# Optimization experiments

Hardware: AMD Instinct MI355X
Metric: run time of the kernel (lower is better)

Reference implementation:

```python
import jax, jax.numpy as jnp
import numpy as np

B, N, D = 8, 4096, 1024
NC, NU = 8, 32            # core / universal experts (num_experts=16, occ_factor=1/4)
E = NC + NU               # 40 total experts
S = 2                     # slots per expert
HC, HU = 4 * D, D         # core hidden = 4*dim, occ hidden = 4*occ_factor*dim = dim
L2_EPS = 1e-6
LN_EPS = 1e-5


def l2norm(x):
    n = jnp.sqrt(jnp.sum(x * x, axis=-1, keepdims=True))
    return x * (1.0 / (n + L2_EPS))


def layernorm(x, g, b):
    mu = jnp.mean(x, axis=-1, keepdims=True)
    var = jnp.mean((x - mu) ** 2, axis=-1, keepdims=True)
    return (x - mu) / jnp.sqrt(var + LN_EPS) * g + b


def entmax15(z):
    # exact 1.5-entmax over last axis (sorted algorithm, Peters et al. 2019)
    z = z / 2.0
    z = z - jnp.max(z, axis=-1, keepdims=True)
    zs = -jnp.sort(-z, axis=-1)                      # descending
    K = z.shape[-1]
    k = jnp.arange(1, K + 1, dtype=z.dtype)
    mean = jnp.cumsum(zs, axis=-1) / k
    meansq = jnp.cumsum(zs * zs, axis=-1) / k
    ss = k * (meansq - mean * mean)
    delta = jnp.maximum((1.0 - ss) / k, 1e-12)
    tau = mean - jnp.sqrt(delta)
    support = jnp.sum((tau <= zs).astype(jnp.int32), axis=-1, keepdims=True)
    tau_star = jnp.take_along_axis(tau, support - 1, axis=-1)
    return jnp.maximum(z - tau_star, 0.0) ** 2


def setup_inputs() -> dict:
    key = jax.random.key(0)
    ks = jax.random.split(key, 8)
    return {
        "x": jax.random.normal(ks[0], (B, N, D), jnp.float32),
        "attn_weight": jax.random.uniform(ks[1], (B, 128), jnp.float32),
        "phi": jax.random.normal(ks[2], (E, S, D), jnp.float32) * 0.02,
        "key_gamma": jnp.ones((D,), jnp.float32),
        "key_beta": jnp.zeros((D,), jnp.float32),
        "query_gamma": jnp.ones((D,), jnp.float32),
        "query_beta": jnp.zeros((D,), jnp.float32),
        "ln_gamma": jnp.ones((D,), jnp.float32),
        "ln_beta": jnp.zeros((D,), jnp.float32),
        "scale0": jnp.asarray(0.5, jnp.float32),
        "scale1": jnp.asarray(0.5, jnp.float32),
        "core_w1": jax.random.normal(ks[3], (NC, D, HC), jnp.float32) * (D ** -0.5),
        "core_b1": jnp.zeros((NC, HC), jnp.float32),
        "core_w2": jax.random.normal(ks[4], (NC, HC, D), jnp.float32) * (HC ** -0.5),
        "core_b2": jnp.zeros((NC, D), jnp.float32),
        "occ_w1": jax.random.normal(ks[5], (NU, D, HU), jnp.float32) * (D ** -0.5),
        "occ_b1": jnp.zeros((NU, HU), jnp.float32),
        "occ_w2": jax.random.normal(ks[6], (NU, HU, D), jnp.float32) * (HU ** -0.5),
        "occ_b2": jnp.zeros((NU, D), jnp.float32),
    }


def _expert_mlp(s, w1, b1, w2, b2):
    # s: [b, e, s, d]; per-expert 2-layer MLP with exact GELU
    h = jax.nn.gelu(jnp.einsum('besd,edh->besh', s, w1) + b1[None, :, None, :], approximate=False)
    return jnp.einsum('besh,ehd->besd', h, w2) + b2[None, :, None, :]


def reference(x, attn_weight, phi, key_gamma, key_beta, query_gamma, query_beta,
              ln_gamma, ln_beta, scale0, scale1,
              core_w1, core_b1, core_w2, core_b2,
              occ_w1, occ_b1, occ_w2, occ_b2):
    # keys: OffsetScale then l2norm
    k = l2norm(x * key_gamma + key_beta)
    # queries: OffsetScale -> LayerNorm -> l2norm on phi
    q = layernorm(phi * query_gamma + query_beta, ln_gamma, ln_beta)
    q = l2norm(q)
    logits = jnp.einsum('bnd,esd->bnes', k, q)                      # [B,N,E,S]
    core_mask = (jnp.arange(E) < NC)[None, None, :, None]
    adjusted = jnp.where(core_mask, logits, jnp.asarray(-10000.0, logits.dtype))
    dispatch = jax.nn.softmax(adjusted / scale0, axis=2)            # softmax over experts
    combine = entmax15((adjusted / scale1).reshape(B, N, E * S))    # [B,N,E*S]
    slots = jnp.einsum('bnd,bnes->besd', x, dispatch)               # [B,E,S,D]
    core_out = _expert_mlp(slots[:, :NC], core_w1, core_b1, core_w2, core_b2)
    occ_out = _expert_mlp(slots[:, NC:], occ_w1, occ_b1, occ_w2, occ_b2)
    out = jnp.concatenate([core_out, occ_out], axis=1).reshape(B, E * S, D)
    return jnp.einsum('bsd,bns->bnd', out, combine)                 # [B,N,D]
```

## Files before the change

### kernel.cpp

```cpp
#include <hip/hip_runtime.h>
#include <hip/hip_bf16.h>

#define B_ 8
#define N_ 4096
#define D_ 1024

#define AS1 __attribute__((address_space(1)))
#define AS3 __attribute__((address_space(3)))
__device__ __forceinline__ void gld16(const float* g, float* l) {
    __builtin_amdgcn_global_load_lds((const AS1 void*)g, (AS3 void*)l, 16, 0, 0);
}

__global__ __launch_bounds__(64) void k_prep(
    const float* __restrict__ phi, const float* __restrict__ qg, const float* __restrict__ qb,
    const float* __restrict__ lng, const float* __restrict__ lnb,
    const float* __restrict__ kg, const float* __restrict__ kb,
    float* __restrict__ qk, float* __restrict__ cj, float* __restrict__ wbuf)
{
    int r = blockIdx.x;
    int lane = threadIdx.x;
    if (r == 16) {
        float cacc = 0.f;
#pragma unroll
        for (int c = 0; c < 16; ++c) {
            int i = c * 64 + lane;
            float g = kg[i], b = kb[i];
            wbuf[i] = g * g;
            wbuf[1024 + i] = 2.0f * g * b;
            cacc += b * b;
        }
#pragma unroll
        for (int m = 32; m; m >>= 1) cacc += __shfl_xor(cacc, m);
        if (lane == 0) wbuf[2048] = cacc;
        return;
    }
    const float* pr = phi + (size_t)r * D_;
    float v[16];
    float s1 = 0.f;
#pragma unroll
    for (int c = 0; c < 16; ++c) {
        int i = c * 64 + lane;
        v[c] = pr[i] * qg[i] + qb[i];
        s1 += v[c];
    }
#pragma unroll
    for (int m = 32; m; m >>= 1) s1 += __shfl_xor(s1, m);
    float mu = s1 * (1.0f / D_);
    float s2 = 0.f;
#pragma unroll
    for (int c = 0; c < 16; ++c) { float dd = v[c] - mu; s2 += dd * dd; }
#pragma unroll
    for (int m = 32; m; m >>= 1) s2 += __shfl_xor(s2, m);
    float var = s2 * (1.0f / D_);
    float inv = 1.0f / sqrtf(var + 1e-5f);
    float u[16];
    float s3 = 0.f;
#pragma unroll
    for (int c = 0; c < 16; ++c) {
        int i = c * 64 + lane;
        u[c] = (v[c] - mu) * inv * lng[i] + lnb[i];
        s3 += u[c] * u[c];
    }
#pragma unroll
    for (int m = 32; m; m >>= 1) s3 += __shfl_xor(s3, m);
    float rn = 1.0f / (sqrtf(s3) + 1e-6f);
    float cacc = 0.f;
#pragma unroll
    for (int c = 0; c < 16; ++c) {
        int i = c * 64 + lane;
        float qv = u[c] * rn;
        qk[(size_t)r * D_ + i] = qv * kg[i];
        cacc += qv * kb[i];
    }
#pragma unroll
    for (int m = 32; m; m >>= 1) cacc += __shfl_xor(cacc, m);
    if (lane == 0) cj[r] = cacc;
}

__global__ __launch_bounds__(256) void k_logits(
    const float* __restrict__ x, const float* __restrict__ qk,
    const float* __restrict__ wbuf, float* __restrict__ lgbuf)
{
    __shared__ float smem[5248];
    float* xs  = smem;
    float* qs  = smem + 4096;
    float* wsd = smem + 5120;

    int tid = threadIdx.x;
    int tok0 = blockIdx.x * 64;
    int tok32 = tid & 31, gg = tid >> 5;
    int wid = tid >> 6;

    float acc[2][17];
#pragma unroll
    for (int u = 0; u < 2; ++u)
#pragma unroll
        for (int v = 0; v < 17; ++v) acc[u][v] = 0.f;

    int st[4], sg[4];
#pragma unroll
    for (int i = 0; i < 4; ++i) {
        int s = i * 256 + tid;
        int tok = s >> 4, sc = s & 15;
        st[i] = tok;
        sg[i] = (sc ^ (tok & 15)) << 2;
    }

#pragma unroll 1
    for (int dc = 0; dc < 16; ++dc) {
#pragma unroll
        for (int i = 0; i < 4; ++i)
            gld16(x + (size_t)(tok0 + st[i]) * D_ + dc * 64 + sg[i],
                  &xs[(i * 256 + wid * 64) * 4]);
        gld16(qk + (size_t)(tid >> 4) * D_ + dc * 64 + ((tid & 15) << 2),
              &qs[wid * 256]);
        if (tid < 128) wsd[tid] = wbuf[(size_t)(tid >> 6) * 1024 + dc * 64 + (tid & 63)];
        __syncthreads();

        const float* qp = qs + gg * 8;
        const float* wp = wsd + gg * 8;
#pragma unroll
        for (int dl4 = 0; dl4 < 2; ++dl4) {
            int c = gg * 2 + dl4;
            int t0 = tok32, t1 = 32 + tok32;
            float4 xv0 = *(const float4*)(&xs[(t0 * 16 + (c ^ (t0 & 15))) * 4]);
            float4 xv1 = *(const float4*)(&xs[(t1 * 16 + (c ^ (t1 & 15))) * 4]);
            float4 w2v = *(const float4*)(wp + dl4 * 4);
            float4 w1v = *(const float4*)(wp + 64 + dl4 * 4);
            acc[0][16] += (w2v.x * xv0.x + w1v.x) * xv0.x + (w2v.y * xv0.y + w1v.y) * xv0.y
                        + (w2v.z * xv0.z + w1v.z) * xv0.z + (w2v.w * xv0.w + w1v.w) * xv0.w;
            acc[1][16] += (w2v.x * xv1.x + w1v.x) * xv1.x + (w2v.y * xv1.y + w1v.y) * xv1.y
                        + (w2v.z * xv1.z + w1v.z) * xv1.z + (w2v.w * xv1.w + w1v.w) * xv1.w;
#pragma unroll
            for (int j = 0; j < 16; ++j) {
                float4 q4 = *(const float4*)(qp + j * 64 + dl4 * 4);
                acc[0][j] += xv0.x * q4.x + xv0.y * q4.y + xv0.z * q4.z + xv0.w * q4.w;
                acc[1][j] += xv1.x * q4.x + xv1.y * q4.y + xv1.z * q4.z + xv1.w * q4.w;
            }
        }
        __syncthreads();
    }

    float* red = smem;
#pragma unroll
    for (int half = 0; half < 2; ++half) {
        __syncthreads();
#pragma unroll
        for (int v = 0; v < 17; ++v) red[(tok32 * 17 + v) * 8 + gg] = acc[half][v];
        __syncthreads();
#pragma unroll
        for (int it = 0; it < 3; ++it) {
            int idx = tid + it * 256;
            if (idx < 544) {
                float4 p0 = *(const float4*)(red + idx * 8);
                float4 p1v = *(const float4*)(red + idx * 8 + 4);
                float sum = ((p0.x + p0.y) + (p0.z + p0.w)) + ((p1v.x + p1v.y) + (p1v.z + p1v.w));
                int t = idx / 17, v = idx - t * 17;
                lgbuf[(size_t)(tok0 + half * 32 + t) * 20 + v] = sum;
            }
        }
    }
}

__global__ __launch_bounds__(64) void k_epi(
    const float* __restrict__ lgbuf, const float* __restrict__ cj,
    const float* __restrict__ wbuf,
    const float* __restrict__ s0p, const float* __restrict__ s1p,
    float* __restrict__ combine, float* __restrict__ dispatch)
{
    int tok = blockIdx.x * 64 + threadIdx.x;
    const float* lp = lgbuf + (size_t)tok * 20;
    float s[17];
    float4 q0 = *(const float4*)(lp + 0);
    float4 q1 = *(const float4*)(lp + 4);
    float4 q2 = *(const float4*)(lp + 8);
    float4 q3 = *(const float4*)(lp + 12);
    s[0] = q0.x; s[1] = q0.y; s[2] = q0.z; s[3] = q0.w;
    s[4] = q1.x; s[5] = q1.y; s[6] = q1.z; s[7] = q1.w;
    s[8] = q2.x; s[9] = q2.y; s[10] = q2.z; s[11] = q2.w;
    s[12] = q3.x; s[13] = q3.y; s[14] = q3.z; s[15] = q3.w;
    s[16] = lp[16];

    float ss = s[16] + wbuf[2048];
    float rn = 1.0f / (sqrtf(ss) + 1e-6f);
    float inv0 = 1.0f / s0p[0];
    float inv1h = 0.5f / s1p[0];
    float lg[16];
#pragma unroll
    for (int j = 0; j < 16; ++j) lg[j] = (s[j] + cj[j]) * rn;

    float dsp[16];
#pragma unroll
    for (int sl = 0; sl < 2; ++sl) {
        float a[8], m = -1e30f;
#pragma unroll
        for (int ee = 0; ee < 8; ++ee) { a[ee] = lg[2 * ee + sl] * inv0; m = fmaxf(m, a[ee]); }
        float den = 0.f;
#pragma unroll
        for (int ee = 0; ee < 8; ++ee) { a[ee] = expf(a[ee] - m); den += a[ee]; }
        float r = 1.0f / den;
#pragma unroll
        for (int ee = 0; ee < 8; ++ee) dsp[2 * ee + sl] = a[ee] * r;
    }

    float z[16], zmax = -1e30f;
#pragma unroll
    for (int j = 0; j < 16; ++j) { z[j] = lg[j] * inv1h; zmax = fmaxf(zmax, z[j]); }
#pragma unroll
    for (int j = 0; j < 16; ++j) z[j] -= zmax;
    float zsr[16];
#pragma unroll
    for (int j = 0; j < 16; ++j) zsr[j] = z[j];
#pragma unroll
    for (int rr = 0; rr < 16; ++rr) {
#pragma unroll
        for (int jj = (rr & 1); jj + 1 < 16; jj += 2) {
            float aa = zsr[jj], bb = zsr[jj + 1];
            zsr[jj] = fmaxf(aa, bb);
            zsr[jj + 1] = fminf(aa, bb);
        }
    }
    float cs = 0.f, css = 0.f, tau_star = 0.f;
#pragma unroll
    for (int kk = 1; kk <= 16; ++kk) {
        cs += zsr[kk - 1];
        css += zsr[kk - 1] * zsr[kk - 1];
        float fk = (float)kk;
        float mean = cs / fk, msq = css / fk;
        float ssv = fk * (msq - mean * mean);
        float delta = fmaxf((1.0f - ssv) / fk, 1e-12f);
        float tau = mean - sqrtf(delta);
        tau_star = (tau <= zsr[kk - 1]) ? tau : tau_star;
    }
    float4* cw = (float4*)(combine + (size_t)tok * 16);
    float4* dw = (float4*)(dispatch + (size_t)tok * 16);
#pragma unroll
    for (int q4i = 0; q4i < 4; ++q4i) {
        float4 cv, dv;
        float t0 = fmaxf(z[q4i * 4 + 0] - tau_star, 0.f);
        float t1 = fmaxf(z[q4i * 4 + 1] - tau_star, 0.f);
        float t2 = fmaxf(z[q4i * 4 + 2] - tau_star, 0.f);
        float t3 = fmaxf(z[q4i * 4 + 3] - tau_star, 0.f);
        cv.x = t0 * t0; cv.y = t1 * t1; cv.z = t2 * t2; cv.w = t3 * t3;
        dv.x = dsp[q4i * 4 + 0]; dv.y = dsp[q4i * 4 + 1];
        dv.z = dsp[q4i * 4 + 2]; dv.w = dsp[q4i * 4 + 3];
        cw[q4i] = cv;
        dw[q4i] = dv;
    }
}

__global__ __launch_bounds__(256) void k_slots_partial(
    const float* __restrict__ x, const float* __restrict__ dispatch,
    float* __restrict__ spart)
{
    __shared__ float sm[1024];
    int nc = blockIdx.x, b = blockIdx.y;
    int tid = threadIdx.x;
    int n0 = nc * 64;
    ((float4*)sm)[tid] = ((const float4*)(dispatch + ((size_t)b * N_ + n0) * 16))[tid];
    __syncthreads();

    const float* xp = x + ((size_t)b * N_ + n0) * D_ + tid * 4;
    float4 acc[16];
#pragma unroll
    for (int j = 0; j < 16; ++j) { acc[j].x = 0.f; acc[j].y = 0.f; acc[j].z = 0.f; acc[j].w = 0.f; }
#pragma unroll 8
    for (int n = 0; n < 64; ++n) {
        float4 xv = *(const float4*)(xp + (size_t)n * D_);
        const float4* q4 = (const float4*)(sm + n * 16);
        float4 s0 = q4[0], s1 = q4[1], s2 = q4[2], s3 = q4[3];
        acc[0].x  += s0.x * xv.x; acc[0].y  += s0.x * xv.y; acc[0].z  += s0.x * xv.z; acc[0].w  += s0.x * xv.w;
        acc[1].x  += s0.y * xv.x; acc[1].y  += s0.y * xv.y; acc[1].z  += s0.y * xv.z; acc[1].w  += s0.y * xv.w;
        acc[2].x  += s0.z * xv.x; acc[2].y  += s0.z * xv.y; acc[2].z  += s0.z * xv.z; acc[2].w  += s0.z * xv.w;
        acc[3].x  += s0.w * xv.x; acc[3].y  += s0.w * xv.y; acc[3].z  += s0.w * xv.z; acc[3].w  += s0.w * xv.w;
        acc[4].x  += s1.x * xv.x; acc[4].y  += s1.x * xv.y; acc[4].z  += s1.x * xv.z; acc[4].w  += s1.x * xv.w;
        acc[5].x  += s1.y * xv.x; acc[5].y  += s1.y * xv.y; acc[5].z  += s1.y * xv.z; acc[5].w  += s1.y * xv.w;
        acc[6].x  += s1.z * xv.x; acc[6].y  += s1.z * xv.y; acc[6].z  += s1.z * xv.z; acc[6].w  += s1.z * xv.w;
        acc[7].x  += s1.w * xv.x; acc[7].y  += s1.w * xv.y; acc[7].z  += s1.w * xv.z; acc[7].w  += s1.w * xv.w;
        acc[8].x  += s2.x * xv.x; acc[8].y  += s2.x * xv.y; acc[8].z  += s2.x * xv.z; acc[8].w  += s2.x * xv.w;
        acc[9].x  += s2.y * xv.x; acc[9].y  += s2.y * xv.y; acc[9].z  += s2.y * xv.z; acc[9].w  += s2.y * xv.w;
        acc[10].x += s2.z * xv.x; acc[10].y += s2.z * xv.y; acc[10].z += s2.z * xv.z; acc[10].w += s2.z * xv.w;
        acc[11].x += s2.w * xv.x; acc[11].y += s2.w * xv.y; acc[11].z += s2.w * xv.z; acc[11].w += s2.w * xv.w;
        acc[12].x += s3.x * xv.x; acc[12].y += s3.x * xv.y; acc[12].z += s3.x * xv.z; acc[12].w += s3.x * xv.w;
        acc[13].x += s3.y * xv.x; acc[13].y += s3.y * xv.y; acc[13].z += s3.y * xv.z; acc[13].w += s3.y * xv.w;
        acc[14].x += s3.z * xv.x; acc[14].y += s3.z * xv.y; acc[14].z += s3.z * xv.z; acc[14].w += s3.z * xv.w;
        acc[15].x += s3.w * xv.x; acc[15].y += s3.w * xv.y; acc[15].z += s3.w * xv.z; acc[15].w += s3.w * xv.w;
    }
    float* op = spart + (((size_t)b * 64 + nc) * 16) * 1024 + tid * 4;
#pragma unroll
    for (int j = 0; j < 16; ++j)
        *(float4*)(op + (size_t)j * 1024) = acc[j];
}

__global__ __launch_bounds__(256) void k_slots_reduce(
    const float* __restrict__ spart, float* __restrict__ slotsT)
{
    int j = blockIdx.x, b = blockIdx.y;
    int tid = threadIdx.x;
    const float* p = spart + ((size_t)(b * 64) * 16 + j) * 1024 + tid * 4;
    float4 s; s.x = 0.f; s.y = 0.f; s.z = 0.f; s.w = 0.f;
#pragma unroll 8
    for (int nc = 0; nc < 64; ++nc) {
        float4 v = *(const float4*)(p + (size_t)nc * 16384);
        s.x += v.x; s.y += v.y; s.z += v.z; s.w += v.w;
    }
    int e = j >> 1, sl = j & 1;
    int t = b * 2 + sl;
    float* o = slotsT + ((size_t)e * 1024 + tid * 4) * 16 + t;
    o[0] = s.x; o[16] = s.y; o[32] = s.z; o[48] = s.w;
}

__global__ __launch_bounds__(256) void k_mlp1(
    const float* __restrict__ w1, const float* __restrict__ slotsT,
    float* __restrict__ p1)
{
    __shared__ float sm[1024];
    int cc = blockIdx.x, ks = blockIdx.y, e = blockIdx.z;
    int tid = threadIdx.x;
    int k0 = ks * 64;
    int col = cc * 1024 + tid * 4;
    ((float4*)sm)[tid] = ((const float4*)(slotsT + ((size_t)e * 1024 + k0) * 16))[tid];
    __syncthreads();

    const float* wp = w1 + (size_t)e * 1024 * 4096 + (size_t)k0 * 4096 + col;
    float4 acc[16];
#pragma unroll
    for (int t = 0; t < 16; ++t) { acc[t].x = 0.f; acc[t].y = 0.f; acc[t].z = 0.f; acc[t].w = 0.f; }
#pragma unroll 8
    for (int kk = 0; kk < 64; ++kk) {
        float4 w = *(const float4*)(wp + (size_t)kk * 4096);
        const float4* q4 = (const float4*)(sm + kk * 16);
        float4 s0 = q4[0], s1 = q4[1], s2 = q4[2], s3 = q4[3];
        acc[0].x  += s0.x * w.x; acc[0].y  += s0.x * w.y; acc[0].z  += s0.x * w.z; acc[0].w  += s0.x * w.w;
        acc[1].x  += s0.y * w.x; acc[1].y  += s0.y * w.y; acc[1].z  += s0.y * w.z; acc[1].w  += s0.y * w.w;
        acc[2].x  += s0.z * w.x; acc[2].y  += s0.z * w.y; acc[2].z  += s0.z * w.z; acc[2].w  += s0.z * w.w;
        acc[3].x  += s0.w * w.x; acc[3].y  += s0.w * w.y; acc[3].z  += s0.w * w.z; acc[3].w  += s0.w * w.w;
        acc[4].x  += s1.x * w.x; acc[4].y  += s1.x * w.y; acc[4].z  += s1.x * w.z; acc[4].w  += s1.x * w.w;
        acc[5].x  += s1.y * w.x; acc[5].y  += s1.y * w.y; acc[5].z  += s1.y * w.z; acc[5].w  += s1.y * w.w;
        acc[6].x  += s1.z * w.x; acc[6].y  += s1.z * w.y; acc[6].z  += s1.z * w.z; acc[6].w  += s1.z * w.w;
        acc[7].x  += s1.w * w.x; acc[7].y  += s1.w * w.y; acc[7].z  += s1.w * w.z; acc[7].w  += s1.w * w.w;
        acc[8].x  += s2.x * w.x; acc[8].y  += s2.x * w.y; acc[8].z  += s2.x * w.z; acc[8].w  += s2.x * w.w;
        acc[9].x  += s2.y * w.x; acc[9].y  += s2.y * w.y; acc[9].z  += s2.y * w.z; acc[9].w  += s2.y * w.w;
        acc[10].x += s2.z * w.x; acc[10].y += s2.z * w.y; acc[10].z += s2.z * w.z; acc[10].w += s2.z * w.w;
        acc[11].x += s2.w * w.x; acc[11].y += s2.w * w.y; acc[11].z += s2.w * w.z; acc[11].w += s2.w * w.w;
        acc[12].x += s3.x * w.x; acc[12].y += s3.x * w.y; acc[12].z += s3.x * w.z; acc[12].w += s3.x * w.w;
        acc[13].x += s3.y * w.x; acc[13].y += s3.y * w.y; acc[13].z += s3.y * w.z; acc[13].w += s3.y * w.w;
        acc[14].x += s3.z * w.x; acc[14].y += s3.z * w.y; acc[14].z += s3.z * w.z; acc[14].w += s3.z * w.w;
        acc[15].x += s3.w * w.x; acc[15].y += s3.w * w.y; acc[15].z += s3.w * w.z; acc[15].w += s3.w * w.w;
    }
    float av0[16], av1[16], av2[16], av3[16];
#pragma unroll
    for (int t = 0; t < 16; ++t) { av0[t] = acc[t].x; av1[t] = acc[t].y; av2[t] = acc[t].z; av3[t] = acc[t].w; }
    float* op = p1 + (((size_t)ks * 8 + e) * 4096 + col) * 16;
#pragma unroll
    for (int q = 0; q < 4; ++q) {
        *(float4*)(op + 0 * 16 + q * 4) = make_float4(av0[q*4+0], av0[q*4+1], av0[q*4+2], av0[q*4+3]);
        *(float4*)(op + 1 * 16 + q * 4) = make_float4(av1[q*4+0], av1[q*4+1], av1[q*4+2], av1[q*4+3]);
        *(float4*)(op + 2 * 16 + q * 4) = make_float4(av2[q*4+0], av2[q*4+1], av2[q*4+2], av2[q*4+3]);
        *(float4*)(op + 3 * 16 + q * 4) = make_float4(av3[q*4+0], av3[q*4+1], av3[q*4+2], av3[q*4+3]);
    }
}

__global__ __launch_bounds__(256) void k_mlp2f(
    const float* __restrict__ w2, const float* __restrict__ p1,
    const float* __restrict__ b1, float* __restrict__ p2)
{
    __shared__ float sm[1024];
    int ks = blockIdx.x, e = blockIdx.y;
    int tid = threadIdx.x;
    int k0 = ks * 64;
    int col = tid * 4;

    {
        int fidx = tid;
        const float* pp = p1 + (size_t)e * 65536 + (size_t)k0 * 16 + fidx * 4;
        float4 s; s.x = 0.f; s.y = 0.f; s.z = 0.f; s.w = 0.f;
#pragma unroll
        for (int ksp = 0; ksp < 16; ++ksp) {
            float4 v = *(const float4*)(pp + (size_t)ksp * 524288);
            s.x += v.x; s.y += v.y; s.z += v.z; s.w += v.w;
        }
        int colh = k0 + (fidx >> 2);
        float bb = b1[(size_t)e * 4096 + colh];
        s.x += bb; s.y += bb; s.z += bb; s.w += bb;
        s.x = 0.5f * s.x * (1.0f + erff(s.x * 0.70710678118654752f));
        s.y = 0.5f * s.y * (1.0f + erff(s.y * 0.70710678118654752f));
        s.z = 0.5f * s.z * (1.0f + erff(s.z * 0.70710678118654752f));
        s.w = 0.5f * s.w * (1.0f + erff(s.w * 0.70710678118654752f));
        *(float4*)(&sm[fidx * 4]) = s;
    }
    __syncthreads();

    const float* wp = w2 + (size_t)e * 4096 * 1024 + (size_t)k0 * 1024 + col;
    float4 acc[16];
#pragma unroll
    for (int t = 0; t < 16; ++t) { acc[t].x = 0.f; acc[t].y = 0.f; acc[t].z = 0.f; acc[t].w = 0.f; }
#pragma unroll 8
    for (int kk = 0; kk < 64; ++kk) {
        float4 w = *(const float4*)(wp + (size_t)kk * 1024);
        const float4* q4 = (const float4*)(sm + kk * 16);
        float4 s0 = q4[0], s1 = q4[1], s2 = q4[2], s3 = q4[3];
        acc[0].x  += s0.x * w.x; acc[0].y  += s0.x * w.y; acc[0].z  += s0.x * w.z; acc[0].w  += s0.x * w.w;
        acc[1].x  += s0.y * w.x; acc[1].y  += s0.y * w.y; acc[1].z  += s0.y * w.z; acc[1].w  += s0.y * w.w;
        acc[2].x  += s0.z * w.x; acc[2].y  += s0.z * w.y; acc[2].z  += s0.z * w.z; acc[2].w  += s0.z * w.w;
        acc[3].x  += s0.w * w.x; acc[3].y  += s0.w * w.y; acc[3].z  += s0.w * w.z; acc[3].w  += s0.w * w.w;
        acc[4].x  += s1.x * w.x; acc[4].y  += s1.x * w.y; acc[4].z  += s1.x * w.z; acc[4].w  += s1.x * w.w;
        acc[5].x  += s1.y * w.x; acc[5].y  += s1.y * w.y; acc[5].z  += s1.y * w.z; acc[5].w  += s1.y * w.w;
        acc[6].x  += s1.z * w.x; acc[6].y  += s1.z * w.y; acc[6].z  += s1.z * w.z; acc[6].w  += s1.z * w.w;
        acc[7].x  += s1.w * w.x; acc[7].y  += s1.w * w.y; acc[7].z  += s1.w * w.z; acc[7].w  += s1.w * w.w;
        acc[8].x  += s2.x * w.x; acc[8].y  += s2.x * w.y; acc[8].z  += s2.x * w.z; acc[8].w  += s2.x * w.w;
        acc[9].x  += s2.y * w.x; acc[9].y  += s2.y * w.y; acc[9].z  += s2.y * w.z; acc[9].w  += s2.y * w.w;
        acc[10].x += s2.z * w.x; acc[10].y += s2.z * w.y; acc[10].z += s2.z * w.z; acc[10].w += s2.z * w.w;
        acc[11].x += s2.w * w.x; acc[11].y += s2.w * w.y; acc[11].z += s2.w * w.z; acc[11].w += s2.w * w.w;
        acc[12].x += s3.x * w.x; acc[12].y += s3.x * w.y; acc[12].z += s3.x * w.z; acc[12].w += s3.x * w.w;
        acc[13].x += s3.y * w.x; acc[13].y += s3.y * w.y; acc[13].z += s3.y * w.z; acc[13].w += s3.y * w.w;
        acc[14].x += s3.z * w.x; acc[14].y += s3.z * w.y; acc[14].z += s3.z * w.z; acc[14].w += s3.z * w.w;
        acc[15].x += s3.w * w.x; acc[15].y += s3.w * w.y; acc[15].z += s3.w * w.z; acc[15].w += s3.w * w.w;
    }
    float av0[16], av1[16], av2[16], av3[16];
#pragma unroll
    for (int t = 0; t < 16; ++t) { av0[t] = acc[t].x; av1[t] = acc[t].y; av2[t] = acc[t].z; av3[t] = acc[t].w; }
    float* op = p2 + (((size_t)ks * 8 + e) * 1024 + col) * 16;
#pragma unroll
    for (int q = 0; q < 4; ++q) {
        *(float4*)(op + 0 * 16 + q * 4) = make_float4(av0[q*4+0], av0[q*4+1], av0[q*4+2], av0[q*4+3]);
        *(float4*)(op + 1 * 16 + q * 4) = make_float4(av1[q*4+0], av1[q*4+1], av1[q*4+2], av1[q*4+3]);
        *(float4*)(op + 2 * 16 + q * 4) = make_float4(av2[q*4+0], av2[q*4+1], av2[q*4+2], av2[q*4+3]);
        *(float4*)(op + 3 * 16 + q * 4) = make_float4(av3[q*4+0], av3[q*4+1], av3[q*4+2], av3[q*4+3]);
    }
}

__global__ __launch_bounds__(256) void k_red2(
    const float* __restrict__ p2, const float* __restrict__ b2,
    float* __restrict__ co)
{
    int idx = blockIdx.x * 256 + threadIdx.x;
    int q = idx & 3, d = (idx >> 2) & 1023, e = idx >> 12;
    const float* p = p2 + ((size_t)e * 1024 + d) * 16 + q * 4;
    float4 s; s.x = 0.f; s.y = 0.f; s.z = 0.f; s.w = 0.f;
#pragma unroll 8
    for (int ks = 0; ks < 64; ++ks) {
        float4 v = *(const float4*)(p + (size_t)ks * 131072);
        s.x += v.x; s.y += v.y; s.z += v.z; s.w += v.w;
    }
    float bb = b2[(size_t)e * 1024 + d];
    float vv[4] = { s.x + bb, s.y + bb, s.z + bb, s.w + bb };
#pragma unroll
    for (int u = 0; u < 4; ++u) {
        int t = q * 4 + u;
        int b = t >> 1, sl = t & 1;
        co[((size_t)b * 16 + e * 2 + sl) * 1024 + d] = vv[u];
    }
}

__global__ __launch_bounds__(256) void k_out(
    const float* __restrict__ co, const float* __restrict__ combine,
    float* __restrict__ out)
{
    __shared__ float sm[1024];
    int b = blockIdx.y, tile = blockIdx.x;
    int tid = threadIdx.x;
    ((float4*)sm)[tid] = ((const float4*)(combine + ((size_t)b * N_ + tile * 64) * 16))[tid];
    float4 cv[16];
#pragma unroll
    for (int j = 0; j < 16; ++j)
        cv[j] = ((const float4*)(co + ((size_t)b * 16 + j) * 1024))[tid];
    __syncthreads();
    float4* ob = (float4*)(out + ((size_t)b * N_ + tile * 64) * 1024) + tid;
#pragma unroll 2
    for (int it = 0; it < 64; ++it) {
        const float* cm = sm + it * 16;
        float4 acc; acc.x = 0.f; acc.y = 0.f; acc.z = 0.f; acc.w = 0.f;
#pragma unroll
        for (int j = 0; j < 16; ++j) {
            float wj = cm[j];
            acc.x += wj * cv[j].x; acc.y += wj * cv[j].y;
            acc.z += wj * cv[j].z; acc.w += wj * cv[j].w;
        }
        ob[(size_t)it * 256] = acc;
    }
}

extern "C" void kernel_launch(void* const* d_in, const int* in_sizes, int n_in,
                              void* d_out, int out_size, void* d_ws, size_t ws_size,
                              hipStream_t stream)
{
    const float* x   = (const float*)d_in[0];
    const float* phi = (const float*)d_in[2];
    const float* kg  = (const float*)d_in[3];
    const float* kb  = (const float*)d_in[4];
    const float* qg  = (const float*)d_in[5];
    const float* qb  = (const float*)d_in[6];
    const float* lng = (const float*)d_in[7];
    const float* lnb = (const float*)d_in[8];
    const float* s0  = (const float*)d_in[9];
    const float* s1  = (const float*)d_in[10];
    const float* w1  = (const float*)d_in[11];
    const float* b1  = (const float*)d_in[12];
    const float* w2  = (const float*)d_in[13];
    const float* b2  = (const float*)d_in[14];

    float* out = (float*)d_out;
    float* ws  = (float*)d_ws;

    float* qk       = ws;
    float* cj       = qk + 16384;
    float* wbuf     = cj + 16;
    float* combine  = wbuf + 2064;
    float* dispatch = combine + 524288;
    float* slotsT   = dispatch + 524288;
    float* co       = slotsT + 131072;
    float* arenaA   = co + 131072;
    float* arenaB   = arenaA + 8388608;
    float* lgbuf    = arenaA;
    float* spart    = arenaA;
    float* p1       = arenaA;
    float* p2       = arenaB;

    k_prep         <<<dim3(17),        dim3(64),  0, stream>>>(phi, qg, qb, lng, lnb, kg, kb, qk, cj, wbuf);
    k_logits       <<<dim3(512),       dim3(256), 0, stream>>>(x, qk, wbuf, lgbuf);
    k_epi          <<<dim3(512),       dim3(64),  0, stream>>>(lgbuf, cj, wbuf, s0, s1, combine, dispatch);
    k_slots_partial<<<dim3(64, 8),     dim3(256), 0, stream>>>(x, dispatch, spart);
    k_slots_reduce <<<dim3(16, 8),     dim3(256), 0, stream>>>(spart, slotsT);
    k_mlp1         <<<dim3(4, 16, 8),  dim3(256), 0, stream>>>(w1, slotsT, p1);
    k_mlp2f        <<<dim3(64, 8),     dim3(256), 0, stream>>>(w2, p1, b1, p2);
    k_red2         <<<dim3(128),       dim3(256), 0, stream>>>(p2, b2, co);
    k_out          <<<dim3(64, 8),     dim3(256), 0, stream>>>(co, combine, out);
}
```

Baseline: 224.0 us.

## Fuse dispatch softmax and slot accumulation into the logits kernel

The logits kernel now computes the dispatch softmax for its 64 tokens in shared memory and immediately accumulates the slot partial sums from the same token tile of x. This removes the separate slots-partial kernel, the dispatch buffer round trip through global memory, and a second pass over x, which can now hit in cache. The cost is a larger shared-memory footprint and more registers in the fused kernel, which may lower occupancy. The logits buffer is moved out of the shared arena so it does not alias the slot partial output.

```diff
diff --git a/kernel.cpp b/kernel.cpp
--- a/kernel.cpp
+++ b/kernel.cpp
@@ -77,14 +77,18 @@
     if (lane == 0) cj[r] = cacc;
 }
 
-__global__ __launch_bounds__(256) void k_logits(
+__global__ __launch_bounds__(256) void k_fused(
     const float* __restrict__ x, const float* __restrict__ qk,
-    const float* __restrict__ wbuf, float* __restrict__ lgbuf)
-{
-    __shared__ float smem[5248];
-    float* xs  = smem;
-    float* qs  = smem + 4096;
-    float* wsd = smem + 5120;
+    const float* __restrict__ wbuf, const float* __restrict__ cj,
+    const float* __restrict__ s0p,
+    float* __restrict__ lgbuf, float* __restrict__ spart)
+{
+    __shared__ float smem[6336];
+    float* xs   = smem;
+    float* qs   = smem + 4096;
+    float* wsd  = smem + 5120;
+    float* sums = smem + 5248;
+    float* disp = smem + 4096;
 
     int tid = threadIdx.x;
     int tok0 = blockIdx.x * 64;
@@ -157,16 +161,76 @@
                 float sum = ((p0.x + p0.y) + (p0.z + p0.w)) + ((p1v.x + p1v.y) + (p1v.z + p1v.w));
                 int t = idx / 17, v = idx - t * 17;
                 lgbuf[(size_t)(tok0 + half * 32 + t) * 20 + v] = sum;
+                sums[(half * 32 + t) * 17 + v] = sum;
             }
         }
     }
+    __syncthreads();
+
+    if (tid < 64) {
+        const float* sp = sums + tid * 17;
+        float ss = sp[16] + wbuf[2048];
+        float rn = 1.0f / (sqrtf(ss) + 1e-6f);
+        float inv0 = 1.0f / s0p[0];
+        float lg[16];
+#pragma unroll
+        for (int j = 0; j < 16; ++j) lg[j] = (sp[j] + cj[j]) * rn;
+        float dsp[16];
+#pragma unroll
+        for (int sl = 0; sl < 2; ++sl) {
+            float a[8], m = -1e30f;
+#pragma unroll
+            for (int ee = 0; ee < 8; ++ee) { a[ee] = lg[2 * ee + sl] * inv0; m = fmaxf(m, a[ee]); }
+            float den = 0.f;
+#pragma unroll
+            for (int ee = 0; ee < 8; ++ee) { a[ee] = expf(a[ee] - m); den += a[ee]; }
+            float r = 1.0f / den;
+#pragma unroll
+            for (int ee = 0; ee < 8; ++ee) dsp[2 * ee + sl] = a[ee] * r;
+        }
+#pragma unroll
+        for (int q4i = 0; q4i < 4; ++q4i)
+            *(float4*)(&disp[tid * 16 + q4i * 4]) =
+                make_float4(dsp[q4i * 4 + 0], dsp[q4i * 4 + 1], dsp[q4i * 4 + 2], dsp[q4i * 4 + 3]);
+    }
+    __syncthreads();
+
+    const float* xp = x + (size_t)tok0 * D_ + tid * 4;
+    float4 acc2[16];
+#pragma unroll
+    for (int j = 0; j < 16; ++j) { acc2[j].x = 0.f; acc2[j].y = 0.f; acc2[j].z = 0.f; acc2[j].w = 0.f; }
+#pragma unroll 8
+    for (int n = 0; n < 64; ++n) {
+        float4 xv = *(const float4*)(xp + (size_t)n * D_);
+        const float4* q4 = (const float4*)(disp + n * 16);
+        float4 s0 = q4[0], s1 = q4[1], s2 = q4[2], s3 = q4[3];
+        acc2[0].x  += s0.x * xv.x; acc2[0].y  += s0.x * xv.y; acc2[0].z  += s0.x * xv.z; acc2[0].w  += s0.x * xv.w;
+        acc2[1].x  += s0.y * xv.x; acc2[1].y  += s0.y * xv.y; acc2[1].z  += s0.y * xv.z; acc2[1].w  += s0.y * xv.w;
+        acc2[2].x  += s0.z * xv.x; acc2[2].y  += s0.z * xv.y; acc2[2].z  += s0.z * xv.z; acc2[2].w  += s0.z * xv.w;
+        acc2[3].x  += s0.w * xv.x; acc2[3].y  += s0.w * xv.y; acc2[3].z  += s0.w * xv.z; acc2[3].w  += s0.w * xv.w;
+        acc2[4].x  += s1.x * xv.x; acc2[4].y  += s1.x * xv.y; acc2[4].z  += s1.x * xv.z; acc2[4].w  += s1.x * xv.w;
+        acc2[5].x  += s1.y * xv.x; acc2[5].y  += s1.y * xv.y; acc2[5].z  += s1.y * xv.z; acc2[5].w  += s1.y * xv.w;
+        acc2[6].x  += s1.z * xv.x; acc2[6].y  += s1.z * xv.y; acc2[6].z  += s1.z * xv.z; acc2[6].w  += s1.z * xv.w;
+        acc2[7].x  += s1.w * xv.x; acc2[7].y  += s1.w * xv.y; acc2[7].z  += s1.w * xv.z; acc2[7].w  += s1.w * xv.w;
+        acc2[8].x  += s2.x * xv.x; acc2[8].y  += s2.x * xv.y; acc2[8].z  += s2.x * xv.z; acc2[8].w  += s2.x * xv.w;
+        acc2[9].x  += s2.y * xv.x; acc2[9].y  += s2.y * xv.y; acc2[9].z  += s2.y * xv.z; acc2[9].w  += s2.y * xv.w;
+        acc2[10].x += s2.z * xv.x; acc2[10].y += s2.z * xv.y; acc2[10].z += s2.z * xv.z; acc2[10].w += s2.z * xv.w;
+        acc2[11].x += s2.w * xv.x; acc2[11].y += s2.w * xv.y; acc2[11].z += s2.w * xv.z; acc2[11].w += s2.w * xv.w;
+        acc2[12].x += s3.x * xv.x; acc2[12].y += s3.x * xv.y; acc2[12].z += s3.x * xv.z; acc2[12].w += s3.x * xv.w;
+        acc2[13].x += s3.y * xv.x; acc2[13].y += s3.y * xv.y; acc2[13].z += s3.y * xv.z; acc2[13].w += s3.y * xv.w;
+        acc2[14].x += s3.z * xv.x; acc2[14].y += s3.z * xv.y; acc2[14].z += s3.z * xv.z; acc2[14].w += s3.z * xv.w;
+        acc2[15].x += s3.w * xv.x; acc2[15].y += s3.w * xv.y; acc2[15].z += s3.w * xv.z; acc2[15].w += s3.w * xv.w;
+    }
+    float* op = spart + ((size_t)blockIdx.x * 16) * 1024 + tid * 4;
+#pragma unroll
+    for (int j = 0; j < 16; ++j)
+        *(float4*)(op + (size_t)j * 1024) = acc2[j];
 }
 
 __global__ __launch_bounds__(64) void k_epi(
     const float* __restrict__ lgbuf, const float* __restrict__ cj,
-    const float* __restrict__ wbuf,
-    const float* __restrict__ s0p, const float* __restrict__ s1p,
-    float* __restrict__ combine, float* __restrict__ dispatch)
+    const float* __restrict__ wbuf, const float* __restrict__ s1p,
+    float* __restrict__ combine)
 {
     int tok = blockIdx.x * 64 + threadIdx.x;
     const float* lp = lgbuf + (size_t)tok * 20;
@@ -183,25 +247,10 @@
 
     float ss = s[16] + wbuf[2048];
     float rn = 1.0f / (sqrtf(ss) + 1e-6f);
-    float inv0 = 1.0f / s0p[0];
     float inv1h = 0.5f / s1p[0];
     float lg[16];
 #pragma unroll
     for (int j = 0; j < 16; ++j) lg[j] = (s[j] + cj[j]) * rn;
-
-    float dsp[16];
-#pragma unroll
-    for (int sl = 0; sl < 2; ++sl) {
-        float a[8], m = -1e30f;
-#pragma unroll
-        for (int ee = 0; ee < 8; ++ee) { a[ee] = lg[2 * ee + sl] * inv0; m = fmaxf(m, a[ee]); }
-        float den = 0.f;
-#pragma unroll
-        for (int ee = 0; ee < 8; ++ee) { a[ee] = expf(a[ee] - m); den += a[ee]; }
-        float r = 1.0f / den;
-#pragma unroll
-        for (int ee = 0; ee < 8; ++ee) dsp[2 * ee + sl] = a[ee] * r;
-    }
 
     float z[16], zmax = -1e30f;
 #pragma unroll
@@ -233,63 +282,16 @@
         tau_star = (tau <= zsr[kk - 1]) ? tau : tau_star;
     }
     float4* cw = (float4*)(combine + (size_t)tok * 16);
-    float4* dw = (float4*)(dispatch + (size_t)tok * 16);
 #pragma unroll
     for (int q4i = 0; q4i < 4; ++q4i) {
-        float4 cv, dv;
+        float4 cv;
         float t0 = fmaxf(z[q4i * 4 + 0] - tau_star, 0.f);
         float t1 = fmaxf(z[q4i * 4 + 1] - tau_star, 0.f);
         float t2 = fmaxf(z[q4i * 4 + 2] - tau_star, 0.f);
         float t3 = fmaxf(z[q4i * 4 + 3] - tau_star, 0.f);
         cv.x = t0 * t0; cv.y = t1 * t1; cv.z = t2 * t2; cv.w = t3 * t3;
-        dv.x = dsp[q4i * 4 + 0]; dv.y = dsp[q4i * 4 + 1];
-        dv.z = dsp[q4i * 4 + 2]; dv.w = dsp[q4i * 4 + 3];
         cw[q4i] = cv;
-        dw[q4i] = dv;
-    }
-}
-
-__global__ __launch_bounds__(256) void k_slots_partial(
-    const float* __restrict__ x, const float* __restrict__ dispatch,
-    float* __restrict__ spart)
-{
-    __shared__ float sm[1024];
-    int nc = blockIdx.x, b = blockIdx.y;
-    int tid = threadIdx.x;
-    int n0 = nc * 64;
-    ((float4*)sm)[tid] = ((const float4*)(dispatch + ((size_t)b * N_ + n0) * 16))[tid];
-    __syncthreads();
-
-    const float* xp = x + ((size_t)b * N_ + n0) * D_ + tid * 4;
-    float4 acc[16];
-#pragma unroll
-    for (int j = 0; j < 16; ++j) { acc[j].x = 0.f; acc[j].y = 0.f; acc[j].z = 0.f; acc[j].w = 0.f; }
-#pragma unroll 8
-    for (int n = 0; n < 64; ++n) {
-        float4 xv = *(const float4*)(xp + (size_t)n * D_);
-        const float4* q4 = (const float4*)(sm + n * 16);
-        float4 s0 = q4[0], s1 = q4[1], s2 = q4[2], s3 = q4[3];
-        acc[0].x  += s0.x * xv.x; acc[0].y  += s0.x * xv.y; acc[0].z  += s0.x * xv.z; acc[0].w  += s0.x * xv.w;
-        acc[1].x  += s0.y * xv.x; acc[1].y  += s0.y * xv.y; acc[1].z  += s0.y * xv.z; acc[1].w  += s0.y * xv.w;
-        acc[2].x  += s0.z * xv.x; acc[2].y  += s0.z * xv.y; acc[2].z  += s0.z * xv.z; acc[2].w  += s0.z * xv.w;
-        acc[3].x  += s0.w * xv.x; acc[3].y  += s0.w * xv.y; acc[3].z  += s0.w * xv.z; acc[3].w  += s0.w * xv.w;
-        acc[4].x  += s1.x * xv.x; acc[4].y  += s1.x * xv.y; acc[4].z  += s1.x * xv.z; acc[4].w  += s1.x * xv.w;
-        acc[5].x  += s1.y * xv.x; acc[5].y  += s1.y * xv.y; acc[5].z  += s1.y * xv.z; acc[5].w  += s1.y * xv.w;
-        acc[6].x  += s1.z * xv.x; acc[6].y  += s1.z * xv.y; acc[6].z  += s1.z * xv.z; acc[6].w  += s1.z * xv.w;
-        acc[7].x  += s1.w * xv.x; acc[7].y  += s1.w * xv.y; acc[7].z  += s1.w * xv.z; acc[7].w  += s1.w * xv.w;
-        acc[8].x  += s2.x * xv.x; acc[8].y  += s2.x * xv.y; acc[8].z  += s2.x * xv.z; acc[8].w  += s2.x * xv.w;
-        acc[9].x  += s2.y * xv.x; acc[9].y  += s2.y * xv.y; acc[9].z  += s2.y * xv.z; acc[9].w  += s2.y * xv.w;
-        acc[10].x += s2.z * xv.x; acc[10].y += s2.z * xv.y; acc[10].z += s2.z * xv.z; acc[10].w += s2.z * xv.w;
-        acc[11].x += s2.w * xv.x; acc[11].y += s2.w * xv.y; acc[11].z += s2.w * xv.z; acc[11].w += s2.w * xv.w;
-        acc[12].x += s3.x * xv.x; acc[12].y += s3.x * xv.y; acc[12].z += s3.x * xv.z; acc[12].w += s3.x * xv.w;
-        acc[13].x += s3.y * xv.x; acc[13].y += s3.y * xv.y; acc[13].z += s3.y * xv.z; acc[13].w += s3.y * xv.w;
-        acc[14].x += s3.z * xv.x; acc[14].y += s3.z * xv.y; acc[14].z += s3.z * xv.z; acc[14].w += s3.z * xv.w;
-        acc[15].x += s3.w * xv.x; acc[15].y += s3.w * xv.y; acc[15].z += s3.w * xv.z; acc[15].w += s3.w * xv.w;
-    }
-    float* op = spart + (((size_t)b * 64 + nc) * 16) * 1024 + tid * 4;
-#pragma unroll
-    for (int j = 0; j < 16; ++j)
-        *(float4*)(op + (size_t)j * 1024) = acc[j];
+    }
 }
 
 __global__ __launch_bounds__(256) void k_slots_reduce(
@@ -507,23 +509,21 @@
     float* cj       = qk + 16384;
     float* wbuf     = cj + 16;
     float* combine  = wbuf + 2064;
-    float* dispatch = combine + 524288;
-    float* slotsT   = dispatch + 524288;
+    float* slotsT   = combine + 524288;
     float* co       = slotsT + 131072;
-    float* arenaA   = co + 131072;
+    float* lgbuf    = co + 131072;
+    float* arenaA   = lgbuf + 655360;
     float* arenaB   = arenaA + 8388608;
-    float* lgbuf    = arenaA;
     float* spart    = arenaA;
     float* p1       = arenaA;
     float* p2       = arenaB;
 
-    k_prep         <<<dim3(17),        dim3(64),  0, stream>>>(phi, qg, qb, lng, lnb, kg, kb, qk, cj, wbuf);
-    k_logits       <<<dim3(512),       dim3(256), 0, stream>>>(x, qk, wbuf, lgbuf);
-    k_epi          <<<dim3(512),       dim3(64),  0, stream>>>(lgbuf, cj, wbuf, s0, s1, combine, dispatch);
-    k_slots_partial<<<dim3(64, 8),     dim3(256), 0, stream>>>(x, dispatch, spart);
-    k_slots_reduce <<<dim3(16, 8),     dim3(256), 0, stream>>>(spart, slotsT);
-    k_mlp1         <<<dim3(4, 16, 8),  dim3(256), 0, stream>>>(w1, slotsT, p1);
-    k_mlp2f        <<<dim3(64, 8),     dim3(256), 0, stream>>>(w2, p1, b1, p2);
-    k_red2         <<<dim3(128),       dim3(256), 0, stream>>>(p2, b2, co);
-    k_out          <<<dim3(64, 8),     dim3(256), 0, stream>>>(co, combine, out);
-}
+    k_prep        <<<dim3(17),        dim3(64),  0, stream>>>(phi, qg, qb, lng, lnb, kg, kb, qk, cj, wbuf);
+    k_fused       <<<dim3(512),       dim3(256), 0, stream>>>(x, qk, wbuf, cj, s0, lgbuf, spart);
+    k_epi         <<<dim3(512),       dim3(64),  0, stream>>>(lgbuf, cj, wbuf, s1, combine);
+    k_slots_reduce<<<dim3(16, 8),     dim3(256), 0, stream>>>(spart, slotsT);
+    k_mlp1        <<<dim3(4, 16, 8),  dim3(256), 0, stream>>>(w1, slotsT, p1);
+    k_mlp2f       <<<dim3(64, 8),     dim3(256), 0, stream>>>(w2, p1, b1, p2);
+    k_red2        <<<dim3(128),       dim3(256), 0, stream>>>(p2, b2, co);
+    k_out         <<<dim3(64, 8),     dim3(256), 0, stream>>>(co, combine, out);
+}
```

After: 217.6 us. -2.9%, faster.
